# Kernel optimization log

Hardware: AMD Instinct MI355X
Metric: run time of the kernel (lower is better)

The kernel has to match this reference:

```python
import math
import jax, jax.numpy as jnp
import numpy as np

N_FFT = 4096
HOP = 1024


def _build_filters(n_fft=N_FFT):
    """Windowed, normalized DFT filters matching the torch module's buffers.
    Returns cos_filters, sin_filters each of shape (n_fft//2+1, 1, n_fft)."""
    n_freqs = n_fft // 2 + 1
    k = np.arange(n_freqs, dtype=np.float64)[:, None]
    n = np.arange(n_fft, dtype=np.float64)[None, :]
    angles = 2.0 * np.pi * k * n / n_fft
    # torch.hann_window(n_fft) is periodic: 0.5 - 0.5*cos(2*pi*n/n_fft)
    window = 0.5 - 0.5 * np.cos(2.0 * np.pi * np.arange(n_fft) / n_fft)
    norm = 1.0 / math.sqrt(n_fft)
    cos_f = (np.cos(angles) * window * norm)[:, None, :].astype(np.float32)
    sin_f = (-np.sin(angles) * window * norm)[:, None, :].astype(np.float32)
    return jnp.asarray(cos_f), jnp.asarray(sin_f)


def setup_inputs() -> dict:
    key = jax.random.key(0)
    x = jax.random.normal(key, (4, 2, 441000), dtype=jnp.float32)  # (B, C, frames)
    cos_filters, sin_filters = _build_filters()
    return {"x": x, "cos_filters": cos_filters, "sin_filters": sin_filters}


def reference(x, cos_filters, sin_filters):
    n_fft = cos_filters.shape[-1]
    hop = HOP
    b, c, frames = x.shape
    xf = x.reshape(b * c, frames)
    pad = n_fft // 2
    xf = jnp.pad(xf, ((0, 0), (pad, pad)), mode="reflect")  # center=True, reflect
    xf = xf[:, None, :]  # (BC, 1, L)
    dn = jax.lax.conv_dimension_numbers(xf.shape, cos_filters.shape, ("NCW", "OIW", "NCW"))
    real = jax.lax.conv_general_dilated(xf, cos_filters, (hop,), "VALID", dimension_numbers=dn)
    imag = jax.lax.conv_general_dilated(xf, sin_filters, (hop,), "VALID", dimension_numbers=dn)
    spec = jnp.stack([real, imag], axis=-1)  # (BC, n_freqs, time_steps, 2)
    n_freqs, time_steps = spec.shape[1], spec.shape[2]
    return spec.reshape(b, c, n_freqs, time_steps, 2)
```

## Files before the change

### kernel.cpp

```cpp
#include <hip/hip_runtime.h>
#include <hip/hip_bf16.h>

#define HOP    1024
#define NFREQ  2049
#define NTIME  431
#define SIGLEN 441000
#define N_REAL 3448
#define MH     1025
#define KH     1088
#define NT2    17
#define NTT    34
#define M_PADH 1152
#define MBLK2  9
#define N_PAD2 3456
#define NBLK2  27
#define NPAIR2 (MBLK2 * NBLK2)
#define MGRP   136

typedef unsigned short ushort_t;
typedef unsigned int   uint_t;
typedef __attribute__((ext_vector_type(8))) __bf16 bf16x8;
typedef __attribute__((ext_vector_type(4))) float  f32x4;

__device__ __forceinline__ ushort_t f2bf(float f) {
    uint_t u = __builtin_bit_cast(uint_t, f);
    u = (u + 0x7FFFu + ((u >> 16) & 1u)) >> 16;
    return (ushort_t)u;
}

__device__ __forceinline__ float frame_sample(const float* __restrict__ xs, int pos) {
    if (pos < 0) pos = -pos;
    else if (pos >= SIGLEN) pos = 2 * SIGLEN - 2 - pos;
    return xs[pos];
}

__device__ __forceinline__ float filt_val(int g, int k, int n) {
    float r = (float)(k * n) * (1.0f / 4096.0f);
    r -= floorf(r);
    const float w = 0.5f - 0.5f * cospif((float)n * (1.0f / 2048.0f));
    const float t = g ? -sinpif(2.0f * r) : cospif(2.0f * r);
    return t * w * 0.015625f;
}

__global__ __launch_bounds__(256) void build_prep(
        const float* __restrict__ x,
        ushort_t* __restrict__ Aall, ushort_t* __restrict__ Ball) {
    const long TA = 2L * M_PADH * MGRP;
    const long TB = (long)N_PAD2 * MGRP;
    const long stride = (long)gridDim.x * blockDim.x;
    for (long task = (long)blockIdx.x * blockDim.x + threadIdx.x; task < TA + TB; task += stride) {
        if (task < TA) {
            const int g  = (int)(task / (M_PADH * MGRP));
            const int r  = (int)(task - (long)g * (M_PADH * MGRP));
            const int k  = r / MGRP;
            const int mg = r - k * MGRP;
            const int m0 = mg * 8;
            alignas(16) ushort_t ve[8], vo[8];
            #pragma unroll
            for (int j = 0; j < 8; ++j) { ve[j] = 0; vo[j] = 0; }
            if (k < MH) {
                #pragma unroll
                for (int j = 0; j < 8; ++j) {
                    const int m = m0 + j;
                    if (m <= 1024) ve[j] = f2bf(filt_val(g, k, 2 * m));
                    if (m <= 1023) vo[j] = f2bf(filt_val(g, k, 2 * m + 1));
                }
            }
            const long dst = ((long)(g * 2) * M_PADH + k) * KH + m0;
            *reinterpret_cast<uint4*>(Aall + dst) = *reinterpret_cast<const uint4*>(ve);
            *reinterpret_cast<uint4*>(Aall + dst + (long)M_PADH * KH) = *reinterpret_cast<const uint4*>(vo);
        } else {
            const long r = task - TA;
            const int n  = (int)(r / MGRP);
            const int mg = (int)(r - (long)n * MGRP);
            const int m0 = mg * 8;
            alignas(16) ushort_t ee[8], eo[8], oe[8], oo[8];
            #pragma unroll
            for (int j = 0; j < 8; ++j) { ee[j] = 0; eo[j] = 0; oe[j] = 0; oo[j] = 0; }
            if (n < N_REAL) {
                const int s = n / NTIME;
                const int t = n - s * NTIME;
                const float* xs = x + (long)s * SIGLEN;
                const int base = t * HOP - 2048;
                const bool interior = (t >= 2) && (t <= 428);
                if (interior && mg <= 127) {
                    const float* fp = xs + base + 2 * m0;
                    const float4 f0 = ((const float4*)fp)[0];
                    const float4 f1 = ((const float4*)fp)[1];
                    const float4 f2 = ((const float4*)fp)[2];
                    const float4 f3 = ((const float4*)fp)[3];
                    const float fe[8] = {f0.x,f0.z,f1.x,f1.z,f2.x,f2.z,f3.x,f3.z};
                    const float fo[8] = {f0.y,f0.w,f1.y,f1.w,f2.y,f2.w,f3.y,f3.w};
                    const float* gp = xs + base + 4096 - 2 * m0 - 16;
                    const float4 h0 = ((const float4*)gp)[0];
                    const float4 h1 = ((const float4*)gp)[1];
                    const float4 h2 = ((const float4*)gp)[2];
                    const float4 h3 = ((const float4*)gp)[3];
                    const float h16 = gp[16];
                    const float hh[17] = {h0.x,h0.y,h0.z,h0.w, h1.x,h1.y,h1.z,h1.w,
                                          h2.x,h2.y,h2.z,h2.w, h3.x,h3.y,h3.z,h3.w, h16};
                    #pragma unroll
                    for (int j = 0; j < 8; ++j) {
                        const float me = hh[16 - 2 * j];
                        const float mo = hh[15 - 2 * j];
                        ee[j] = f2bf(fe[j] + me);
                        oe[j] = f2bf(fe[j] - me);
                        eo[j] = f2bf(fo[j] + mo);
                        oo[j] = f2bf(fo[j] - mo);
                    }
                    if (mg == 0) {
                        ee[0] = f2bf(fe[0]);
                        oe[0] = f2bf(fe[0]);
                    }
                } else if (mg <= 128) {
                    #pragma unroll
                    for (int j = 0; j < 8; ++j) {
                        const int m = m0 + j;
                        const int ide = 2 * m;
                        if (m <= 1024) {
                            const float fn = frame_sample(xs, base + ide);
                            const float fm = (ide >= 1 && ide <= 2047) ? frame_sample(xs, base + 4096 - ide) : 0.0f;
                            ee[j] = f2bf(fn + fm);
                            oe[j] = f2bf(fn - fm);
                        }
                        if (m <= 1023) {
                            const int ido = 2 * m + 1;
                            const float gn = frame_sample(xs, base + ido);
                            const float gm = frame_sample(xs, base + 4096 - ido);
                            eo[j] = f2bf(gn + gm);
                            oo[j] = f2bf(gn - gm);
                        }
                    }
                }
            }
            const long MSZ = (long)N_PAD2 * KH;
            const long dst = (long)n * KH + m0;
            *reinterpret_cast<uint4*>(Ball + dst)           = *reinterpret_cast<const uint4*>(ee);
            *reinterpret_cast<uint4*>(Ball + dst + MSZ)     = *reinterpret_cast<const uint4*>(eo);
            *reinterpret_cast<uint4*>(Ball + dst + 2 * MSZ) = *reinterpret_cast<const uint4*>(oe);
            *reinterpret_cast<uint4*>(Ball + dst + 3 * MSZ) = *reinterpret_cast<const uint4*>(oo);
        }
    }
}

__device__ __forceinline__ void gload_lds16(const ushort_t* g, ushort_t* l) {
    __builtin_amdgcn_global_load_lds(
        (const __attribute__((address_space(1))) void*)g,
        (__attribute__((address_space(3))) void*)l,
        16, 0, 0);
}

__device__ __forceinline__ f32x4 MF(bf16x8 x, bf16x8 y, f32x4 c) {
    return __builtin_amdgcn_mfma_f32_16x16x32_bf16(x, y, c, 0, 0, 0);
}

#define SBAR()  __builtin_amdgcn_s_barrier()
#define SCHED() __builtin_amdgcn_sched_barrier(0)

__global__ __launch_bounds__(256, 2) void stft_gemm(
        const ushort_t* __restrict__ Aall, const ushort_t* __restrict__ Ball,
        float* __restrict__ out) {
    __shared__ alignas(16) ushort_t As[2][128 * 64];
    __shared__ alignas(16) ushort_t Bs[2][128 * 64];

    const int pid = blockIdx.x;
    const int xc  = pid & 7;
    const int g   = (pid >> 3) & 1;
    const int i   = pid >> 4;
    const int sz  = (xc < 3) ? 31 : 30;
    if (i >= sz) return;
    const int p   = xc * 30 + ((xc < 3) ? xc : 3) + i;
    const int bm  = p % MBLK2;
    const int bn  = p / MBLK2;

    const int tid  = threadIdx.x;
    const int lane = tid & 63;
    const int wv   = tid >> 6;
    const int wm   = wv & 1;
    const int wn   = wv >> 1;

    const ushort_t* A0 = Aall + (long)(g * 2) * M_PADH * KH;
    const ushort_t* A1 = A0 + (long)M_PADH * KH;
    const ushort_t* B0 = Ball + (long)(g * 2) * N_PAD2 * KH;
    const ushort_t* B1 = B0 + (long)N_PAD2 * KH;

    const long Ar0 = (long)bm * 128;
    const long Br0 = (long)bn * 128;

    const int rb   = tid >> 3;
    const int scol = ((((tid & 7) << 4) ^ ((rb & 7) << 4)) >> 1);
    const int ldsw = wv * 512;

    auto STG = [&](const ushort_t* Gb, long r0, int kcol, ushort_t* dst, int half) {
        const ushort_t* gp = Gb + (r0 + half * 64 + rb) * (long)KH + kcol + scol;
        gload_lds16(gp,                 dst + half * 4096 + ldsw);
        gload_lds16(gp + 32 * (long)KH, dst + half * 4096 + 2048 + ldsw);
    };

    const int lrow = lane & 15;
    const int kq   = (lane >> 4) << 4;
    auto FRAG = [&](const ushort_t* buf, int lr, int kb) -> bf16x8 {
        const char* pp = reinterpret_cast<const char*>(buf)
                        + lr * 128 + ((kb + kq) ^ ((lr & 7) << 4));
        return *reinterpret_cast<const bf16x8*>(pp);
    };

    f32x4 accE[4][4] = {}, accO[4][4] = {};
    bf16x8 a[4][2], b[4][2];
    const int arow = wm * 64 + lrow;
    const int brow = wn * 64 + lrow;

    auto ABK = [&](int j, const ushort_t*& Ab, const ushort_t*& Bb, int& kc) {
        if (j >= NT2) { Ab = A1; Bb = B1; kc = (j - NT2) * 64; }
        else          { Ab = A0; Bb = B0; kc = j * 64; }
    };

    {
        const ushort_t *Ab, *Bb; int kc;
        ABK(0, Ab, Bb, kc);
        STG(Ab, Ar0, kc, As[0], 0); STG(Ab, Ar0, kc, As[0], 1);
        STG(Bb, Br0, kc, Bs[0], 0); STG(Bb, Br0, kc, Bs[0], 1);
        ABK(1, Ab, Bb, kc);
        STG(Ab, Ar0, kc, As[1], 0); STG(Ab, Ar0, kc, As[1], 1);
        STG(Bb, Br0, kc, Bs[1], 0); STG(Bb, Br0, kc, Bs[1], 1);
    }
    asm volatile("s_waitcnt vmcnt(8)" ::: "memory");
    SBAR();

    auto ITER = [&](int t, f32x4 (&acc)[4][4]) {
        const int cur = t & 1;
        const ushort_t* Ac = As[cur];
        const ushort_t* Bc = Bs[cur];

        #pragma unroll
        for (int mf = 0; mf < 4; ++mf) {
            a[mf][0] = FRAG(Ac, arow + mf * 16, 0);
            a[mf][1] = FRAG(Ac, arow + mf * 16, 64);
        }
        #pragma unroll
        for (int nf = 0; nf < 4; ++nf) {
            b[nf][0] = FRAG(Bc, brow + nf * 16, 0);
            b[nf][1] = FRAG(Bc, brow + nf * 16, 64);
        }
        __builtin_amdgcn_s_setprio(1);
        #pragma unroll
        for (int mf = 0; mf < 4; ++mf)
            #pragma unroll
            for (int nf = 0; nf < 4; ++nf) {
                acc[mf][nf] = MF(a[mf][0], b[nf][0], acc[mf][nf]);
                acc[mf][nf] = MF(a[mf][1], b[nf][1], acc[mf][nf]);
            }
        __builtin_amdgcn_s_setprio(0);
        asm volatile("s_waitcnt lgkmcnt(0)" ::: "memory");
        SCHED();
        SBAR();
        if (t + 2 < NTT) {
            const ushort_t *A_2, *B_2; int kc2;
            ABK(t + 2, A_2, B_2, kc2);
            STG(A_2, Ar0, kc2, As[cur], 0); STG(A_2, Ar0, kc2, As[cur], 1);
            STG(B_2, Br0, kc2, Bs[cur], 0); STG(B_2, Br0, kc2, Bs[cur], 1);
            asm volatile("s_waitcnt vmcnt(8)" ::: "memory");
        } else if (t + 1 < NTT) {
            asm volatile("s_waitcnt vmcnt(0)" ::: "memory");
        }
        if (t + 1 < NTT) SBAR();
    };

    for (int t = 0; t < NT2; ++t)   ITER(t, accE);
    for (int t = NT2; t < NTT; ++t) ITER(t, accO);

    const int row_off = (lane >> 4) << 2;
    const int col_off = lane & 15;
    const int kg  = bm * 128 + wm * 64;
    const int ng0 = bn * 128 + wn * 64;

    #pragma unroll
    for (int nf = 0; nf < 4; ++nf) {
        const int ng = ng0 + nf * 16 + col_off;
        if (ng >= N_REAL) continue;
        const int s  = ng / NTIME;
        const int tt = ng - s * NTIME;
        const long rowbase = (long)s * NFREQ * NTIME;
        #pragma unroll
        for (int mf = 0; mf < 4; ++mf) {
            #pragma unroll
            for (int r = 0; r < 4; ++r) {
                const int k = kg + mf * 16 + row_off + r;
                if (k < MH) {
                    const float vE = accE[mf][nf][r];
                    const float vO = accO[mf][nf][r];
                    const float vP = vE + vO;
                    const float vM = g ? (vO - vE) : (vE - vO);
                    out[(rowbase + (long)k * NTIME + tt) * 2 + g]          = vP;
                    out[(rowbase + (long)(2048 - k) * NTIME + tt) * 2 + g] = vM;
                }
            }
        }
    }
}

extern "C" void kernel_launch(void* const* d_in, const int* in_sizes, int n_in,
                              void* d_out, int out_size, void* d_ws, size_t ws_size,
                              hipStream_t stream) {
    const float* x    = (const float*)d_in[0];
    float* out = (float*)d_out;

    ushort_t* Aall = (ushort_t*)d_ws;
    ushort_t* Ball = Aall + 4L * M_PADH * KH;

    build_prep<<<2048, 256, 0, stream>>>(x, Aall, Ball);

    stft_gemm<<<496, 256, 0, stream>>>(Aall, Ball, out);
}
```

Baseline: 75.87 us.

## Split even/odd K halves across wave pairs and load B fragments directly

The B matrix is written by the prep kernel in an MFMA-fragment-tiled layout, so the GEMM loads B operands straight from global memory into registers and stages only A through LDS. The block grows to 512 threads: half the waves accumulate the even half of K and half the odd half, concurrently rather than as two sequential 17-step loops. Their partial sums are combined through LDS in the epilogue. This is meant to halve the serial K loop and LDS traffic, at the cost of uncached-in-LDS global B loads, a full vmcnt(0) wait every iteration, and extra epilogue barriers.

```diff
diff --git a/kernel.cpp b/kernel.cpp
--- a/kernel.cpp
+++ b/kernel.cpp
@@ -8,8 +8,8 @@
 #define N_REAL 3448
 #define MH     1025
 #define KH     1088
+#define KH32   34
 #define NT2    17
-#define NTT    34
 #define M_PADH 1152
 #define MBLK2  9
 #define N_PAD2 3456
@@ -21,6 +21,7 @@
 typedef unsigned int   uint_t;
 typedef __attribute__((ext_vector_type(8))) __bf16 bf16x8;
 typedef __attribute__((ext_vector_type(4))) float  f32x4;
+typedef const __attribute__((address_space(1))) bf16x8* gcv_t;
 
 __device__ __forceinline__ ushort_t f2bf(float f) {
     uint_t u = __builtin_bit_cast(uint_t, f);
@@ -134,11 +135,12 @@
                 }
             }
             const long MSZ = (long)N_PAD2 * KH;
-            const long dst = (long)n * KH + m0;
-            *reinterpret_cast<uint4*>(Ball + dst)           = *reinterpret_cast<const uint4*>(ee);
-            *reinterpret_cast<uint4*>(Ball + dst + MSZ)     = *reinterpret_cast<const uint4*>(eo);
-            *reinterpret_cast<uint4*>(Ball + dst + 2 * MSZ) = *reinterpret_cast<const uint4*>(oe);
-            *reinterpret_cast<uint4*>(Ball + dst + 3 * MSZ) = *reinterpret_cast<const uint4*>(oo);
+            const long foff = ((long)(n >> 4) * KH32 + (m0 >> 5)) * 512
+                            + (long)(((((m0 >> 3) & 3) << 4) | (n & 15)) * 8);
+            *reinterpret_cast<uint4*>(Ball + foff)           = *reinterpret_cast<const uint4*>(ee);
+            *reinterpret_cast<uint4*>(Ball + foff + MSZ)     = *reinterpret_cast<const uint4*>(eo);
+            *reinterpret_cast<uint4*>(Ball + foff + 2 * MSZ) = *reinterpret_cast<const uint4*>(oe);
+            *reinterpret_cast<uint4*>(Ball + foff + 3 * MSZ) = *reinterpret_cast<const uint4*>(oo);
         }
     }
 }
@@ -157,11 +159,10 @@
 #define SBAR()  __builtin_amdgcn_s_barrier()
 #define SCHED() __builtin_amdgcn_sched_barrier(0)
 
-__global__ __launch_bounds__(256, 2) void stft_gemm(
+__global__ __launch_bounds__(512, 4) void stft_gemm(
         const ushort_t* __restrict__ Aall, const ushort_t* __restrict__ Ball,
         float* __restrict__ out) {
-    __shared__ alignas(16) ushort_t As[2][128 * 64];
-    __shared__ alignas(16) ushort_t Bs[2][128 * 64];
+    __shared__ alignas(16) ushort_t LDSBUF[4 * 8192];
 
     const int pid = blockIdx.x;
     const int xc  = pid & 7;
@@ -176,25 +177,33 @@
     const int tid  = threadIdx.x;
     const int lane = tid & 63;
     const int wv   = tid >> 6;
-    const int wm   = wv & 1;
-    const int wn   = wv >> 1;
+    const int par  = wv & 1;
+    const int q    = wv >> 1;
+    const int wm   = q & 1;
+    const int wn   = q >> 1;
 
     const ushort_t* A0 = Aall + (long)(g * 2) * M_PADH * KH;
     const ushort_t* A1 = A0 + (long)M_PADH * KH;
-    const ushort_t* B0 = Ball + (long)(g * 2) * N_PAD2 * KH;
-    const ushort_t* B1 = B0 + (long)N_PAD2 * KH;
+    const ushort_t* Bmat = Ball + (long)(g * 2 + par) * N_PAD2 * KH;
 
     const long Ar0 = (long)bm * 128;
-    const long Br0 = (long)bn * 128;
 
     const int rb   = tid >> 3;
     const int scol = ((((tid & 7) << 4) ^ ((rb & 7) << 4)) >> 1);
     const int ldsw = wv * 512;
 
-    auto STG = [&](const ushort_t* Gb, long r0, int kcol, ushort_t* dst, int half) {
-        const ushort_t* gp = Gb + (r0 + half * 64 + rb) * (long)KH + kcol + scol;
-        gload_lds16(gp,                 dst + half * 4096 + ldsw);
-        gload_lds16(gp + 32 * (long)KH, dst + half * 4096 + 2048 + ldsw);
+    auto STG1 = [&](const ushort_t* G, long row0, int kc, ushort_t* dst8k) {
+        const ushort_t* gp = G + (row0 + rb) * (long)KH + kc + scol;
+        gload_lds16(gp, dst8k + ldsw);
+    };
+    auto STAGE = [&](int t, int buf) {
+        const int kc = t * 64;
+        ushort_t* de = LDSBUF + buf * 8192;
+        ushort_t* do_ = LDSBUF + (2 + buf) * 8192;
+        STG1(A0, Ar0,      kc, de);
+        STG1(A0, Ar0 + 64, kc, de + 4096);
+        STG1(A1, Ar0,      kc, do_);
+        STG1(A1, Ar0 + 64, kc, do_ + 4096);
     };
 
     const int lrow = lane & 15;
@@ -205,43 +214,35 @@
         return *reinterpret_cast<const bf16x8*>(pp);
     };
 
-    f32x4 accE[4][4] = {}, accO[4][4] = {};
+    f32x4 acc[4][4] = {};
     bf16x8 a[4][2], b[4][2];
     const int arow = wm * 64 + lrow;
-    const int brow = wn * 64 + lrow;
-
-    auto ABK = [&](int j, const ushort_t*& Ab, const ushort_t*& Bb, int& kc) {
-        if (j >= NT2) { Ab = A1; Bb = B1; kc = (j - NT2) * 64; }
-        else          { Ab = A0; Bb = B0; kc = j * 64; }
-    };
-
-    {
-        const ushort_t *Ab, *Bb; int kc;
-        ABK(0, Ab, Bb, kc);
-        STG(Ab, Ar0, kc, As[0], 0); STG(Ab, Ar0, kc, As[0], 1);
-        STG(Bb, Br0, kc, Bs[0], 0); STG(Bb, Br0, kc, Bs[0], 1);
-        ABK(1, Ab, Bb, kc);
-        STG(Ab, Ar0, kc, As[1], 0); STG(Ab, Ar0, kc, As[1], 1);
-        STG(Bb, Br0, kc, Bs[1], 0); STG(Bb, Br0, kc, Bs[1], 1);
-    }
-    asm volatile("s_waitcnt vmcnt(8)" ::: "memory");
+    const ushort_t* AsP = LDSBUF + par * 2 * 8192;
+    const long n16b = (long)(bn * 8 + wn * 4);
+
+    STAGE(0, 0);
+    STAGE(1, 1);
+    asm volatile("s_waitcnt vmcnt(4)" ::: "memory");
     SBAR();
 
-    auto ITER = [&](int t, f32x4 (&acc)[4][4]) {
+    for (int t = 0; t < NT2; ++t) {
         const int cur = t & 1;
-        const ushort_t* Ac = As[cur];
-        const ushort_t* Bc = Bs[cur];
-
+        const ushort_t* Ac = AsP + cur * 8192;
+
+        {
+            const long f0 = (n16b * KH32 + t * 2) << 9;
+            #pragma unroll
+            for (int nf = 0; nf < 4; ++nf) {
+                const ushort_t* bp = Bmat + f0 + (((long)nf * KH32) << 9) + (lane << 3);
+                b[nf][0] = *(gcv_t)bp;
+                b[nf][1] = *(gcv_t)(bp + 512);
+            }
+        }
         #pragma unroll
         for (int mf = 0; mf < 4; ++mf) {
             a[mf][0] = FRAG(Ac, arow + mf * 16, 0);
             a[mf][1] = FRAG(Ac, arow + mf * 16, 64);
         }
-        #pragma unroll
-        for (int nf = 0; nf < 4; ++nf) {
-            b[nf][0] = FRAG(Bc, brow + nf * 16, 0);
-            b[nf][1] = FRAG(Bc, brow + nf * 16, 64);
-        }
         __builtin_amdgcn_s_setprio(1);
         #pragma unroll
         for (int mf = 0; mf < 4; ++mf)
@@ -252,50 +253,61 @@
             }
         __builtin_amdgcn_s_setprio(0);
         asm volatile("s_waitcnt lgkmcnt(0)" ::: "memory");
+        asm volatile("s_waitcnt vmcnt(0)" ::: "memory");
         SCHED();
         SBAR();
-        if (t + 2 < NTT) {
-            const ushort_t *A_2, *B_2; int kc2;
-            ABK(t + 2, A_2, B_2, kc2);
-            STG(A_2, Ar0, kc2, As[cur], 0); STG(A_2, Ar0, kc2, As[cur], 1);
-            STG(B_2, Br0, kc2, Bs[cur], 0); STG(B_2, Br0, kc2, Bs[cur], 1);
-            asm volatile("s_waitcnt vmcnt(8)" ::: "memory");
-        } else if (t + 1 < NTT) {
-            asm volatile("s_waitcnt vmcnt(0)" ::: "memory");
-        }
-        if (t + 1 < NTT) SBAR();
-    };
-
-    for (int t = 0; t < NT2; ++t)   ITER(t, accE);
-    for (int t = NT2; t < NTT; ++t) ITER(t, accO);
-
+        if (t + 2 < NT2) STAGE(t + 2, cur);
+    }
+
+    float* fb   = reinterpret_cast<float*>(LDSBUF);
+    float* qbuf = fb + q * 2176;
     const int row_off = (lane >> 4) << 2;
     const int col_off = lane & 15;
     const int kg  = bm * 128 + wm * 64;
     const int ng0 = bn * 128 + wn * 64;
 
+    SBAR();
     #pragma unroll
-    for (int nf = 0; nf < 4; ++nf) {
-        const int ng = ng0 + nf * 16 + col_off;
-        if (ng >= N_REAL) continue;
-        const int s  = ng / NTIME;
-        const int tt = ng - s * NTIME;
-        const long rowbase = (long)s * NFREQ * NTIME;
-        #pragma unroll
-        for (int mf = 0; mf < 4; ++mf) {
-            #pragma unroll
-            for (int r = 0; r < 4; ++r) {
-                const int k = kg + mf * 16 + row_off + r;
-                if (k < MH) {
-                    const float vE = accE[mf][nf][r];
-                    const float vO = accO[mf][nf][r];
-                    const float vP = vE + vO;
-                    const float vM = g ? (vO - vE) : (vE - vO);
-                    out[(rowbase + (long)k * NTIME + tt) * 2 + g]          = vP;
-                    out[(rowbase + (long)(2048 - k) * NTIME + tt) * 2 + g] = vM;
+    for (int rr = 0; rr < 2; ++rr) {
+        if (par == 0) {
+            #pragma unroll
+            for (int nfr = 0; nfr < 2; ++nfr)
+                #pragma unroll
+                for (int mf = 0; mf < 4; ++mf)
+                    *reinterpret_cast<f32x4*>(&qbuf[(nfr * 16 + col_off) * 68 + mf * 16 + row_off])
+                        = acc[mf][rr * 2 + nfr];
+        }
+        SBAR();
+        if (par == 1) {
+            #pragma unroll
+            for (int nfr = 0; nfr < 2; ++nfr) {
+                const int nf = rr * 2 + nfr;
+                const int ng = ng0 + nf * 16 + col_off;
+                if (ng < N_REAL) {
+                    const int s  = ng / NTIME;
+                    const int tt = ng - s * NTIME;
+                    const long rowbase = (long)s * NFREQ * NTIME;
+                    #pragma unroll
+                    for (int mf = 0; mf < 4; ++mf) {
+                        const f32x4 e = *reinterpret_cast<const f32x4*>(
+                            &qbuf[(nfr * 16 + col_off) * 68 + mf * 16 + row_off]);
+                        #pragma unroll
+                        for (int r4 = 0; r4 < 4; ++r4) {
+                            const int k = kg + mf * 16 + row_off + r4;
+                            if (k < MH) {
+                                const float vE = e[r4];
+                                const float vO = acc[mf][nf][r4];
+                                const float vP = vE + vO;
+                                const float vM = g ? (vO - vE) : (vE - vO);
+                                out[(rowbase + (long)k * NTIME + tt) * 2 + g]          = vP;
+                                out[(rowbase + (long)(2048 - k) * NTIME + tt) * 2 + g] = vM;
+                            }
+                        }
+                    }
                 }
             }
         }
+        SBAR();
     }
 }
 
@@ -310,5 +322,5 @@
 
     build_prep<<<2048, 256, 0, stream>>>(x, Aall, Ball);
 
-    stft_gemm<<<496, 256, 0, stream>>>(Aall, Ball, out);
-}
+    stft_gemm<<<496, 512, 0, stream>>>(Aall, Ball, out);
+}
```

Result: slower. 165.2 us (+117.7%).
